# Optimization experiments

Hardware: AMD Instinct MI355X
Metric: run time of the kernel (lower is better)

Reference implementation:

```python
import jax, jax.numpy as jnp
import numpy as np

N_NODES = 50000


def gcn_conv(x, edge_index, W, b):
    # linear transform: x [N, Fin] @ W.T [Fin, Fout]
    h = x @ W.T
    # message passing: gather from source nodes, scatter-add to targets
    src, dst = edge_index[0], edge_index[1]
    out = jax.ops.segment_sum(h[src], dst, num_segments=N_NODES)
    return out + b


def setup_inputs() -> dict:
    key = jax.random.key(0)
    ks = jax.random.split(key, 5)
    E = 800000
    d_in, d_h, d_out = 128, 128, 40
    scale = lambda fin: 1.0 / np.sqrt(fin)
    return {
        "x": jax.random.normal(ks[0], (N_NODES, d_in), dtype=jnp.float32),
        "edge_index": jax.random.randint(ks[1], (2, E), 0, N_NODES, dtype=jnp.int64),
        "W0": jax.random.normal(ks[2], (d_h, d_in), dtype=jnp.float32) * scale(d_in),
        "b0": jnp.zeros((d_h,), dtype=jnp.float32),
        "W1": jax.random.normal(ks[3], (d_h, d_h), dtype=jnp.float32) * scale(d_h),
        "b1": jnp.zeros((d_h,), dtype=jnp.float32),
        "W2": jax.random.normal(ks[4], (d_out, d_h), dtype=jnp.float32) * scale(d_h),
        "b2": jnp.zeros((d_out,), dtype=jnp.float32),
    }


def reference(x, edge_index, W0, b0, W1, b1, W2, b2):
    h = jax.nn.relu(gcn_conv(x, edge_index, W0, b0))
    h = jax.nn.relu(gcn_conv(h, edge_index, W1, b1))
    return gcn_conv(h, edge_index, W2, b2)
```

## Files before the change

kernel.cpp:

```cpp
#include <hip/hip_runtime.h>

#define N_NODES 50000
#define NB 782
#define PA_CH 4096
#define CAP 2048

typedef __attribute__((ext_vector_type(8))) short bf16x8;
typedef __attribute__((ext_vector_type(4))) float f32x4;

static __device__ __forceinline__ unsigned short f2bf(float f) {
    unsigned int u = __float_as_uint(f);
    u += 0x7fffu + ((u >> 16) & 1u);
    return (unsigned short)(u >> 16);
}
static __device__ __forceinline__ float bfl(unsigned int u) { return __uint_as_float(u << 16); }
static __device__ __forceinline__ float bfh(unsigned int u) { return __uint_as_float(u & 0xffff0000u); }


__global__ void zero_gcnt(int* __restrict__ g) {
    int i = blockIdx.x * 256 + threadIdx.x;
    if (i < NB) g[i] = 0;
}

__global__ __launch_bounds__(256) void bucket_scatter(const int* __restrict__ src,
                                                      const int* __restrict__ dst,
                                                      int* __restrict__ gcnt,
                                                      unsigned* __restrict__ ebuf, int E) {
    __shared__ int cnt[NB];
    __shared__ int run[NB];
    int base = blockIdx.x * PA_CH;
    int end = base + PA_CH; if (end > E) end = E;
    int b4 = base >> 2, e4 = end >> 2;
    for (int i = threadIdx.x; i < NB; i += 256) cnt[i] = 0;
    __syncthreads();
    for (int i = b4 + threadIdx.x; i < e4; i += 256) {
        int4 d = ((const int4*)dst)[i];
        atomicAdd(&cnt[d.x >> 6], 1);
        atomicAdd(&cnt[d.y >> 6], 1);
        atomicAdd(&cnt[d.z >> 6], 1);
        atomicAdd(&cnt[d.w >> 6], 1);
    }
    __syncthreads();
    for (int i = threadIdx.x; i < NB; i += 256) {
        int c = cnt[i];
        run[i] = c ? (i * CAP + atomicAdd(&gcnt[i], c)) : 0;
    }
    __syncthreads();
    for (int i = b4 + threadIdx.x; i < e4; i += 256) {
        int4 d = ((const int4*)dst)[i];
        int4 s = ((const int4*)src)[i];
        int p0 = atomicAdd(&run[d.x >> 6], 1);
        ebuf[p0] = (unsigned)s.x | ((unsigned)(d.x & 63) << 16);
        int p1 = atomicAdd(&run[d.y >> 6], 1);
        ebuf[p1] = (unsigned)s.y | ((unsigned)(d.y & 63) << 16);
        int p2 = atomicAdd(&run[d.z >> 6], 1);
        ebuf[p2] = (unsigned)s.z | ((unsigned)(d.z & 63) << 16);
        int p3 = atomicAdd(&run[d.w >> 6], 1);
        ebuf[p3] = (unsigned)s.w | ((unsigned)(d.w & 63) << 16);
    }
}

__global__ __launch_bounds__(1024) void scan_nb(const int* __restrict__ gcnt,
                                                int* __restrict__ bptr,
                                                int* __restrict__ row_ptr, int E) {
    int tid = threadIdx.x;
    int v = (tid < NB) ? gcnt[tid] : 0;
    int lane = tid & 63, wv = tid >> 6;
    int incl = v;
    for (int off = 1; off < 64; off <<= 1) {
        int t = __shfl_up(incl, off);
        if (lane >= off) incl += t;
    }
    __shared__ int ws[16];
    if (lane == 63) ws[wv] = incl;
    __syncthreads();
    int woff = 0;
    for (int i = 0; i < wv; ++i) woff += ws[i];
    int excl = woff + incl - v;
    if (tid < NB) bptr[tid] = excl;
    if (tid == NB - 1) { bptr[NB] = excl + v; row_ptr[N_NODES] = E; }
}

__global__ __launch_bounds__(256) void bucket_sort(const unsigned* __restrict__ ebuf,
                                                   const int* __restrict__ gcnt,
                                                   const int* __restrict__ bptr,
                                                   unsigned short* __restrict__ edge_src,
                                                   int* __restrict__ row_ptr) {
    int b = blockIdx.x;
    int start = bptr[b];
    int n = gcnt[b]; if (n > CAP) n = CAP;
    const unsigned* slot = ebuf + (size_t)b * CAP;
    __shared__ unsigned raw[CAP];
    __shared__ unsigned grp[CAP];
    __shared__ int bins[64], pref[64], cur[64];
    int tid = threadIdx.x;
    for (int i = tid; i < n; i += 256) raw[i] = slot[i];
    if (tid < 64) bins[tid] = 0;
    __syncthreads();
    for (int i = tid; i < n; i += 256) atomicAdd(&bins[raw[i] >> 16], 1);
    __syncthreads();
    if (tid < 64) {
        int v = bins[tid];
        int incl = v;
        for (int off = 1; off < 64; off <<= 1) {
            int t = __shfl_up(incl, off);
            if (tid >= off) incl += t;
        }
        pref[tid] = incl - v;
        cur[tid] = incl - v;
    }
    __syncthreads();
    for (int i = tid; i < n; i += 256) {
        unsigned r = raw[i];
        int pos = atomicAdd(&cur[r >> 16], 1);
        grp[pos] = r;
    }
    __syncthreads();
    for (int i = tid; i < n; i += 256) {
        unsigned v = grp[i];
        int s = v >> 16;
        int lo = pref[s];
        int len = bins[s];
        int rank = 0;
        for (int j = lo; j < lo + len; ++j) {
            unsigned u = grp[j];
            rank += (u < v) || (u == v && j < i);
        }
        edge_src[start + lo + rank] = (unsigned short)(v & 0xffffu);
    }
    int d0 = b * 64;
    if (tid < 64 && d0 + tid < N_NODES) row_ptr[d0 + tid] = start + pref[tid];
}


__global__ void prep_all(const float* __restrict__ W0, const float* __restrict__ W1,
                         const float* __restrict__ W2, short* __restrict__ Wb) {
    int i = blockIdx.x * 256 + threadIdx.x;
    if (i >= 19 * 2048) return;
    const float* W; int fout; int local;
    if (i < 8 * 2048)       { W = W0; fout = 128; local = i; }
    else if (i < 16 * 2048) { W = W1; fout = 128; local = i - 8 * 2048; }
    else                    { W = W2; fout = 40;  local = i - 16 * 2048; }
    int j = local & 7;
    int l = (local >> 3) & 63;
    int kt = (local >> 9) & 3;
    int ct = local >> 11;
    int col = ct * 16 + (l & 15);
    int k = kt * 32 + (l >> 4) * 8 + j;
    float v = (col < fout) ? W[col * 128 + k] : 0.0f;
    Wb[i] = (short)f2bf(v);
}


template <int FT>
__global__ __launch_bounds__(256) void gemm_mfma(const float* __restrict__ inp,
                                                 const short* __restrict__ Wb,
                                                 unsigned short* __restrict__ out, int fout) {
    const int l = threadIdx.x & 63;
    const int w = threadIdx.x >> 6;
    const int r16 = l & 15;
    const int khalf = l >> 4;
    int rowA = blockIdx.x * 64 + w * 16 + r16;
    if (rowA >= N_NODES) rowA = N_NODES - 1;

    f32x4 acc[FT];
#pragma unroll
    for (int ct = 0; ct < FT; ++ct) acc[ct] = (f32x4){0.f, 0.f, 0.f, 0.f};

#pragma unroll
    for (int kt = 0; kt < 4; ++kt) {
        const float* ip = inp + (size_t)rowA * 128 + kt * 32 + khalf * 8;
        float4 f0 = ((const float4*)ip)[0];
        float4 f1 = ((const float4*)ip)[1];
        bf16x8 a;
        a[0] = (short)f2bf(f0.x); a[1] = (short)f2bf(f0.y);
        a[2] = (short)f2bf(f0.z); a[3] = (short)f2bf(f0.w);
        a[4] = (short)f2bf(f1.x); a[5] = (short)f2bf(f1.y);
        a[6] = (short)f2bf(f1.z); a[7] = (short)f2bf(f1.w);
#pragma unroll
        for (int ct = 0; ct < FT; ++ct) {
            bf16x8 bfr = *(const bf16x8*)(Wb + (((ct * 4 + kt) * 64 + l) * 8));
            acc[ct] = __builtin_amdgcn_mfma_f32_16x16x32_bf16(a, bfr, acc[ct], 0, 0, 0);
        }
    }

    const int rowD0 = blockIdx.x * 64 + w * 16 + khalf * 4;
#pragma unroll
    for (int ct = 0; ct < FT; ++ct) {
        int col = ct * 16 + r16;
#pragma unroll
        for (int rr = 0; rr < 4; ++rr) {
            int row = rowD0 + rr;
            if (row < N_NODES && col < fout)
                out[(size_t)row * fout + col] = f2bf(acc[ct][rr]);
        }
    }
}

template <int NCT>
__global__ __launch_bounds__(256) void gather_gemm(const unsigned short* __restrict__ h,
                                                   const int* __restrict__ row_ptr,
                                                   const unsigned short* __restrict__ es,
                                                   const float* __restrict__ bias,
                                                   const short* __restrict__ Wb,
                                                   unsigned short* __restrict__ out, int fout) {
    __shared__ float agg[16][132];
    const int node0 = blockIdx.x * 16;

    {
        const int nl = threadIdx.x >> 4;
        const int q  = threadIdx.x & 15;
        const int node = node0 + nl;
        int beg = row_ptr[node], end = row_ptr[node + 1];
        float acc[8];
        float4 c0 = ((const float4*)bias)[q * 2];
        float4 c1 = ((const float4*)bias)[q * 2 + 1];
        acc[0] = c0.x; acc[1] = c0.y; acc[2] = c0.z; acc[3] = c0.w;
        acc[4] = c1.x; acc[5] = c1.y; acc[6] = c1.z; acc[7] = c1.w;
        int e = beg;
        for (; e + 1 < end; e += 2) {
            int s0 = es[e], s1 = es[e + 1];
            const uint4 v0 = ((const uint4*)(h + (size_t)s0 * 128))[q];
            const uint4 v1 = ((const uint4*)(h + (size_t)s1 * 128))[q];
            acc[0] += bfl(v0.x); acc[1] += bfh(v0.x);
            acc[2] += bfl(v0.y); acc[3] += bfh(v0.y);
            acc[4] += bfl(v0.z); acc[5] += bfh(v0.z);
            acc[6] += bfl(v0.w); acc[7] += bfh(v0.w);
            acc[0] += bfl(v1.x); acc[1] += bfh(v1.x);
            acc[2] += bfl(v1.y); acc[3] += bfh(v1.y);
            acc[4] += bfl(v1.z); acc[5] += bfh(v1.z);
            acc[6] += bfl(v1.w); acc[7] += bfh(v1.w);
        }
        if (e < end) {
            int s = es[e];
            const uint4 v = ((const uint4*)(h + (size_t)s * 128))[q];
            acc[0] += bfl(v.x); acc[1] += bfh(v.x);
            acc[2] += bfl(v.y); acc[3] += bfh(v.y);
            acc[4] += bfl(v.z); acc[5] += bfh(v.z);
            acc[6] += bfl(v.w); acc[7] += bfh(v.w);
        }
        float* row = &agg[nl][q * 8];
        ((float4*)row)[0] = make_float4(fmaxf(acc[0], 0.f), fmaxf(acc[1], 0.f),
                                        fmaxf(acc[2], 0.f), fmaxf(acc[3], 0.f));
        ((float4*)row)[1] = make_float4(fmaxf(acc[4], 0.f), fmaxf(acc[5], 0.f),
                                        fmaxf(acc[6], 0.f), fmaxf(acc[7], 0.f));
    }
    __syncthreads();

    const int l = threadIdx.x & 63;
    const int w = threadIdx.x >> 6;
    const int r16 = l & 15;
    const int khalf = l >> 4;
    f32x4 acc[(NCT + 3) / 4];
#pragma unroll
    for (int i = 0; i < (NCT + 3) / 4; ++i) acc[i] = (f32x4){0.f, 0.f, 0.f, 0.f};

#pragma unroll
    for (int kt = 0; kt < 4; ++kt) {
        const float* ap = &agg[r16][kt * 32 + khalf * 8];
        float4 f0 = ((const float4*)ap)[0];
        float4 f1 = ((const float4*)ap)[1];
        bf16x8 a;
        a[0] = (short)f2bf(f0.x); a[1] = (short)f2bf(f0.y);
        a[2] = (short)f2bf(f0.z); a[3] = (short)f2bf(f0.w);
        a[4] = (short)f2bf(f1.x); a[5] = (short)f2bf(f1.y);
        a[6] = (short)f2bf(f1.z); a[7] = (short)f2bf(f1.w);
        int i = 0;
#pragma unroll
        for (int ct = w; ct < NCT; ct += 4, ++i) {
            bf16x8 bfr = *(const bf16x8*)(Wb + (((ct * 4 + kt) * 64 + l) * 8));
            acc[i] = __builtin_amdgcn_mfma_f32_16x16x32_bf16(a, bfr, acc[i], 0, 0, 0);
        }
    }

    {
        int i = 0;
#pragma unroll
        for (int ct = w; ct < NCT; ct += 4, ++i) {
            int col = ct * 16 + r16;
            if (col < fout) {
#pragma unroll
                for (int rr = 0; rr < 4; ++rr)
                    out[(size_t)(node0 + khalf * 4 + rr) * fout + col] = f2bf(acc[i][rr]);
            }
        }
    }
}


__global__ void gather_f40_bf(const unsigned short* __restrict__ h,
                              const int* __restrict__ row_ptr,
                              const unsigned short* __restrict__ es,
                              const float* __restrict__ b,
                              float* __restrict__ out) {
    int gid = blockIdx.x * blockDim.x + threadIdx.x;
    int node = gid / 5;
    int q = gid - node * 5;
    if (node >= N_NODES) return;
    int beg = row_ptr[node];
    int end = row_ptr[node + 1];
    float acc[8];
#pragma unroll
    for (int j = 0; j < 8; ++j) acc[j] = b[q * 8 + j];
    int e = beg;
    for (; e + 1 < end; e += 2) {
        int s0 = es[e], s1 = es[e + 1];
        const uint4 v0 = *(const uint4*)(h + (size_t)s0 * 40 + q * 8);
        const uint4 v1 = *(const uint4*)(h + (size_t)s1 * 40 + q * 8);
        acc[0] += bfl(v0.x); acc[1] += bfh(v0.x);
        acc[2] += bfl(v0.y); acc[3] += bfh(v0.y);
        acc[4] += bfl(v0.z); acc[5] += bfh(v0.z);
        acc[6] += bfl(v0.w); acc[7] += bfh(v0.w);
        acc[0] += bfl(v1.x); acc[1] += bfh(v1.x);
        acc[2] += bfl(v1.y); acc[3] += bfh(v1.y);
        acc[4] += bfl(v1.z); acc[5] += bfh(v1.z);
        acc[6] += bfl(v1.w); acc[7] += bfh(v1.w);
    }
    if (e < end) {
        int s = es[e];
        const uint4 v = *(const uint4*)(h + (size_t)s * 40 + q * 8);
        acc[0] += bfl(v.x); acc[1] += bfh(v.x);
        acc[2] += bfl(v.y); acc[3] += bfh(v.y);
        acc[4] += bfl(v.z); acc[5] += bfh(v.z);
        acc[6] += bfl(v.w); acc[7] += bfh(v.w);
    }
    float* o = out + (size_t)node * 40 + q * 8;
    ((float4*)o)[0] = make_float4(acc[0], acc[1], acc[2], acc[3]);
    ((float4*)o)[1] = make_float4(acc[4], acc[5], acc[6], acc[7]);
}


extern "C" void kernel_launch(void* const* d_in, const int* in_sizes, int n_in,
                              void* d_out, int out_size, void* d_ws, size_t ws_size,
                              hipStream_t stream) {
    const float* x  = (const float*)d_in[0];
    const int*   ei = (const int*)d_in[1];
    const float* W0 = (const float*)d_in[2];
    const float* b0 = (const float*)d_in[3];
    const float* W1 = (const float*)d_in[4];
    const float* b1 = (const float*)d_in[5];
    const float* W2 = (const float*)d_in[6];
    const float* b2 = (const float*)d_in[7];
    float* out = (float*)d_out;

    const int E = in_sizes[1] / 2;
    const int* src = ei;
    const int* dst = ei + E;

    char* p = (char*)d_ws;
    unsigned short* hb0 = (unsigned short*)p;  p += (size_t)N_NODES * 128 * 2;
    unsigned short* hb1 = (unsigned short*)p;  p += (size_t)N_NODES * 128 * 2;
    unsigned short* hb2 = (unsigned short*)p;  p += (size_t)N_NODES * 40 * 2;
    short* wb = (short*)p;                     p += 19 * 2048 * 2;
    unsigned* ebuf = (unsigned*)p;             p += (size_t)NB * CAP * 4;
    int* row_ptr = (int*)p;                    p += (N_NODES + 1) * 4;
    int* bptr = (int*)p;                       p += (NB + 1) * 4;
    int* gcnt = (int*)p;                       p += NB * 4;
    unsigned short* edge_src = (unsigned short*)p;

    short* wb0 = wb;
    short* wb1 = wb + 8 * 2048;
    short* wb2 = wb + 16 * 2048;

    zero_gcnt<<<4, 256, 0, stream>>>(gcnt);
    bucket_scatter<<<(E + PA_CH - 1) / PA_CH, 256, 0, stream>>>(src, dst, gcnt, ebuf, E);
    scan_nb<<<1, 1024, 0, stream>>>(gcnt, bptr, row_ptr, E);
    bucket_sort<<<NB, 256, 0, stream>>>(ebuf, gcnt, bptr, edge_src, row_ptr);

    prep_all<<<(19 * 2048 + 255) / 256, 256, 0, stream>>>(W0, W1, W2, wb);

    gemm_mfma<8><<<(N_NODES + 63) / 64, 256, 0, stream>>>(x, wb0, hb0, 128);

    gather_gemm<8><<<N_NODES / 16, 256, 0, stream>>>(hb0, row_ptr, edge_src, b0, wb1, hb1, 128);

    gather_gemm<3><<<N_NODES / 16, 256, 0, stream>>>(hb1, row_ptr, edge_src, b1, wb2, hb2, 40);

    gather_f40_bf<<<(N_NODES * 5 + 255) / 256, 256, 0, stream>>>(hb2, row_ptr, edge_src, b2, out);
}
```

Measured before the change: 124.8 us.

## Merge weight prep with counter zeroing and co-launch bucketing with first GEMM

```diff
diff --git a/kernel.cpp b/kernel.cpp
--- a/kernel.cpp
+++ b/kernel.cpp
@@ -17,48 +17,111 @@
 static __device__ __forceinline__ float bfh(unsigned int u) { return __uint_as_float(u & 0xffff0000u); }
 
 
-__global__ void zero_gcnt(int* __restrict__ g) {
+__global__ void zero_prep(int* __restrict__ g,
+                          const float* __restrict__ W0, const float* __restrict__ W1,
+                          const float* __restrict__ W2, short* __restrict__ Wb) {
     int i = blockIdx.x * 256 + threadIdx.x;
     if (i < NB) g[i] = 0;
-}
-
-__global__ __launch_bounds__(256) void bucket_scatter(const int* __restrict__ src,
-                                                      const int* __restrict__ dst,
-                                                      int* __restrict__ gcnt,
-                                                      unsigned* __restrict__ ebuf, int E) {
+    if (i >= 19 * 2048) return;
+    const float* W; int fout; int local;
+    if (i < 8 * 2048)       { W = W0; fout = 128; local = i; }
+    else if (i < 16 * 2048) { W = W1; fout = 128; local = i - 8 * 2048; }
+    else                    { W = W2; fout = 40;  local = i - 16 * 2048; }
+    int j = local & 7;
+    int l = (local >> 3) & 63;
+    int kt = (local >> 9) & 3;
+    int ct = local >> 11;
+    int col = ct * 16 + (l & 15);
+    int k = kt * 32 + (l >> 4) * 8 + j;
+    float v = (col < fout) ? W[col * 128 + k] : 0.0f;
+    Wb[i] = (short)f2bf(v);
+}
+
+
+__global__ __launch_bounds__(256) void fused_phase1(const int* __restrict__ src,
+                                                    const int* __restrict__ dst,
+                                                    int* __restrict__ gcnt,
+                                                    unsigned* __restrict__ ebuf, int E, int SB,
+                                                    const float* __restrict__ x,
+                                                    const short* __restrict__ wb0,
+                                                    unsigned short* __restrict__ hb0) {
     __shared__ int cnt[NB];
     __shared__ int run[NB];
-    int base = blockIdx.x * PA_CH;
-    int end = base + PA_CH; if (end > E) end = E;
-    int b4 = base >> 2, e4 = end >> 2;
-    for (int i = threadIdx.x; i < NB; i += 256) cnt[i] = 0;
-    __syncthreads();
-    for (int i = b4 + threadIdx.x; i < e4; i += 256) {
-        int4 d = ((const int4*)dst)[i];
-        atomicAdd(&cnt[d.x >> 6], 1);
-        atomicAdd(&cnt[d.y >> 6], 1);
-        atomicAdd(&cnt[d.z >> 6], 1);
-        atomicAdd(&cnt[d.w >> 6], 1);
-    }
-    __syncthreads();
-    for (int i = threadIdx.x; i < NB; i += 256) {
-        int c = cnt[i];
-        run[i] = c ? (i * CAP + atomicAdd(&gcnt[i], c)) : 0;
-    }
-    __syncthreads();
-    for (int i = b4 + threadIdx.x; i < e4; i += 256) {
-        int4 d = ((const int4*)dst)[i];
-        int4 s = ((const int4*)src)[i];
-        int p0 = atomicAdd(&run[d.x >> 6], 1);
-        ebuf[p0] = (unsigned)s.x | ((unsigned)(d.x & 63) << 16);
-        int p1 = atomicAdd(&run[d.y >> 6], 1);
-        ebuf[p1] = (unsigned)s.y | ((unsigned)(d.y & 63) << 16);
-        int p2 = atomicAdd(&run[d.z >> 6], 1);
-        ebuf[p2] = (unsigned)s.z | ((unsigned)(d.z & 63) << 16);
-        int p3 = atomicAdd(&run[d.w >> 6], 1);
-        ebuf[p3] = (unsigned)s.w | ((unsigned)(d.w & 63) << 16);
-    }
-}
+    if (blockIdx.x < (unsigned)SB) {
+        int base = blockIdx.x * PA_CH;
+        int end = base + PA_CH; if (end > E) end = E;
+        int b4 = base >> 2, e4 = end >> 2;
+        for (int i = threadIdx.x; i < NB; i += 256) cnt[i] = 0;
+        __syncthreads();
+        for (int i = b4 + threadIdx.x; i < e4; i += 256) {
+            int4 d = ((const int4*)dst)[i];
+            atomicAdd(&cnt[d.x >> 6], 1);
+            atomicAdd(&cnt[d.y >> 6], 1);
+            atomicAdd(&cnt[d.z >> 6], 1);
+            atomicAdd(&cnt[d.w >> 6], 1);
+        }
+        __syncthreads();
+        for (int i = threadIdx.x; i < NB; i += 256) {
+            int c = cnt[i];
+            run[i] = c ? (i * CAP + atomicAdd(&gcnt[i], c)) : 0;
+        }
+        __syncthreads();
+        for (int i = b4 + threadIdx.x; i < e4; i += 256) {
+            int4 d = ((const int4*)dst)[i];
+            int4 s = ((const int4*)src)[i];
+            int p0 = atomicAdd(&run[d.x >> 6], 1);
+            ebuf[p0] = (unsigned)s.x | ((unsigned)(d.x & 63) << 16);
+            int p1 = atomicAdd(&run[d.y >> 6], 1);
+            ebuf[p1] = (unsigned)s.y | ((unsigned)(d.y & 63) << 16);
+            int p2 = atomicAdd(&run[d.z >> 6], 1);
+            ebuf[p2] = (unsigned)s.z | ((unsigned)(d.z & 63) << 16);
+            int p3 = atomicAdd(&run[d.w >> 6], 1);
+            ebuf[p3] = (unsigned)s.w | ((unsigned)(d.w & 63) << 16);
+        }
+    } else {
+        const int bid = blockIdx.x - SB;
+        const int l = threadIdx.x & 63;
+        const int w = threadIdx.x >> 6;
+        const int r16 = l & 15;
+        const int khalf = l >> 4;
+        int rowA = bid * 64 + w * 16 + r16;
+        if (rowA >= N_NODES) rowA = N_NODES - 1;
+
+        f32x4 acc[8];
+#pragma unroll
+        for (int ct = 0; ct < 8; ++ct) acc[ct] = (f32x4){0.f, 0.f, 0.f, 0.f};
+
+#pragma unroll
+        for (int kt = 0; kt < 4; ++kt) {
+            const float* ip = x + (size_t)rowA * 128 + kt * 32 + khalf * 8;
+            float4 f0 = ((const float4*)ip)[0];
+            float4 f1 = ((const float4*)ip)[1];
+            bf16x8 a;
+            a[0] = (short)f2bf(f0.x); a[1] = (short)f2bf(f0.y);
+            a[2] = (short)f2bf(f0.z); a[3] = (short)f2bf(f0.w);
+            a[4] = (short)f2bf(f1.x); a[5] = (short)f2bf(f1.y);
+            a[6] = (short)f2bf(f1.z); a[7] = (short)f2bf(f1.w);
+#pragma unroll
+            for (int ct = 0; ct < 8; ++ct) {
+                bf16x8 bfr = *(const bf16x8*)(wb0 + (((ct * 4 + kt) * 64 + l) * 8));
+                acc[ct] = __builtin_amdgcn_mfma_f32_16x16x32_bf16(a, bfr, acc[ct], 0, 0, 0);
+            }
+        }
+
+        const int rowD0 = bid * 64 + w * 16 + khalf * 4;
+#pragma unroll
+        for (int ct = 0; ct < 8; ++ct) {
+            int col = ct * 16 + r16;
+#pragma unroll
+            for (int rr = 0; rr < 4; ++rr) {
+                int row = rowD0 + rr;
+                if (row < N_NODES)
+                    hb0[(size_t)row * 128 + col] = f2bf(acc[ct][rr]);
+            }
+        }
+    }
+}
+
 
 __global__ __launch_bounds__(1024) void scan_nb(const int* __restrict__ gcnt,
                                                 int* __restrict__ bptr,
@@ -130,71 +193,6 @@
     }
     int d0 = b * 64;
     if (tid < 64 && d0 + tid < N_NODES) row_ptr[d0 + tid] = start + pref[tid];
-}
-
-
-__global__ void prep_all(const float* __restrict__ W0, const float* __restrict__ W1,
-                         const float* __restrict__ W2, short* __restrict__ Wb) {
-    int i = blockIdx.x * 256 + threadIdx.x;
-    if (i >= 19 * 2048) return;
-    const float* W; int fout; int local;
-    if (i < 8 * 2048)       { W = W0; fout = 128; local = i; }
-    else if (i < 16 * 2048) { W = W1; fout = 128; local = i - 8 * 2048; }
-    else                    { W = W2; fout = 40;  local = i - 16 * 2048; }
-    int j = local & 7;
-    int l = (local >> 3) & 63;
-    int kt = (local >> 9) & 3;
-    int ct = local >> 11;
-    int col = ct * 16 + (l & 15);
-    int k = kt * 32 + (l >> 4) * 8 + j;
-    float v = (col < fout) ? W[col * 128 + k] : 0.0f;
-    Wb[i] = (short)f2bf(v);
-}
-
-
-template <int FT>
-__global__ __launch_bounds__(256) void gemm_mfma(const float* __restrict__ inp,
-                                                 const short* __restrict__ Wb,
-                                                 unsigned short* __restrict__ out, int fout) {
-    const int l = threadIdx.x & 63;
-    const int w = threadIdx.x >> 6;
-    const int r16 = l & 15;
-    const int khalf = l >> 4;
-    int rowA = blockIdx.x * 64 + w * 16 + r16;
-    if (rowA >= N_NODES) rowA = N_NODES - 1;
-
-    f32x4 acc[FT];
-#pragma unroll
-    for (int ct = 0; ct < FT; ++ct) acc[ct] = (f32x4){0.f, 0.f, 0.f, 0.f};
-
-#pragma unroll
-    for (int kt = 0; kt < 4; ++kt) {
-        const float* ip = inp + (size_t)rowA * 128 + kt * 32 + khalf * 8;
-        float4 f0 = ((const float4*)ip)[0];
-        float4 f1 = ((const float4*)ip)[1];
-        bf16x8 a;
-        a[0] = (short)f2bf(f0.x); a[1] = (short)f2bf(f0.y);
-        a[2] = (short)f2bf(f0.z); a[3] = (short)f2bf(f0.w);
-        a[4] = (short)f2bf(f1.x); a[5] = (short)f2bf(f1.y);
-        a[6] = (short)f2bf(f1.z); a[7] = (short)f2bf(f1.w);
-#pragma unroll
-        for (int ct = 0; ct < FT; ++ct) {
-            bf16x8 bfr = *(const bf16x8*)(Wb + (((ct * 4 + kt) * 64 + l) * 8));
-            acc[ct] = __builtin_amdgcn_mfma_f32_16x16x32_bf16(a, bfr, acc[ct], 0, 0, 0);
-        }
-    }
-
-    const int rowD0 = blockIdx.x * 64 + w * 16 + khalf * 4;
-#pragma unroll
-    for (int ct = 0; ct < FT; ++ct) {
-        int col = ct * 16 + r16;
-#pragma unroll
-        for (int rr = 0; rr < 4; ++rr) {
-            int row = rowD0 + rr;
-            if (row < N_NODES && col < fout)
-                out[(size_t)row * fout + col] = f2bf(acc[ct][rr]);
-        }
-    }
 }
 
 template <int NCT>
@@ -362,15 +360,16 @@
     short* wb1 = wb + 8 * 2048;
     short* wb2 = wb + 16 * 2048;
 
-    zero_gcnt<<<4, 256, 0, stream>>>(gcnt);
-    bucket_scatter<<<(E + PA_CH - 1) / PA_CH, 256, 0, stream>>>(src, dst, gcnt, ebuf, E);
+    const int SB = (E + PA_CH - 1) / PA_CH;
+    const int GB = (N_NODES + 63) / 64;
+
+    zero_prep<<<(19 * 2048 + 255) / 256, 256, 0, stream>>>(gcnt, W0, W1, W2, wb);
+
+    fused_phase1<<<SB + GB, 256, 0, stream>>>(src, dst, gcnt, ebuf, E, SB, x, wb0, hb0);
+
     scan_nb<<<1, 1024, 0, stream>>>(gcnt, bptr, row_ptr, E);
     bucket_sort<<<NB, 256, 0, stream>>>(ebuf, gcnt, bptr, edge_src, row_ptr);
 
-    prep_all<<<(19 * 2048 + 255) / 256, 256, 0, stream>>>(W0, W1, W2, wb);
-
-    gemm_mfma<8><<<(N_NODES + 63) / 64, 256, 0, stream>>>(x, wb0, hb0, 128);
-
     gather_gemm<8><<<N_NODES / 16, 256, 0, stream>>>(hb0, row_ptr, edge_src, b0, wb1, hb1, 128);
 
     gather_gemm<3><<<N_NODES / 16, 256, 0, stream>>>(hb1, row_ptr, edge_src, b1, wb2, hb2, 40);
```

After: 116.9 us. -6.3%, faster.
